# Performance work log

Hardware: AMD Instinct MI355X
Metric: run time of the kernel (lower is better)

## Reference

```python
import jax, jax.numpy as jnp
import numpy as np

N_NODES = 100000
N_EDGES = 300000
HIDDEN = 256

def _lin_init(key, fan_in, fan_out):
    return jax.random.normal(key, (fan_in, fan_out), jnp.float32) / np.sqrt(fan_in)

def setup_inputs():
    key = jax.random.key(0)
    ks = jax.random.split(key, 16)
    x = jax.random.randint(ks[0], (N_NODES, 16), 0, 11).astype(jnp.float32)
    edge_index = jax.random.randint(ks[1], (2, N_EDGES), 0, N_NODES)
    edge_attr = jax.random.randint(ks[2], (N_EDGES, 4), 0, 5).astype(jnp.float32)
    batch = jnp.sort(jax.random.randint(ks[3], (N_NODES,), 0, 256))
    atom_emb = jax.random.normal(ks[4], (11, 64), jnp.float32)
    bond_emb_table = jax.random.normal(ks[5], (5, 64), jnp.float32)
    vp_w1 = _lin_init(ks[6], 64, 32); vp_b1 = jnp.zeros((32,), jnp.float32)
    vp_w2 = _lin_init(ks[7], 32, 8)
    # chemical-knowledge bias init: max_valence - 1 for atom types 0..7 (bias dim is 8)
    vp_b2 = jnp.array([3., 2., 1., 5., 0., 0., 0., 0.], jnp.float32)
    gnn_wself = jax.random.normal(ks[8], (3, HIDDEN, HIDDEN), jnp.float32) / np.sqrt(HIDDEN)
    gnn_bself = jnp.zeros((3, HIDDEN), jnp.float32)
    gnn_wmsg = jax.random.normal(ks[9], (3, HIDDEN + 64, HIDDEN), jnp.float32) / np.sqrt(HIDDEN + 64)
    gnn_bmsg = jnp.zeros((3, HIDDEN), jnp.float32)
    bc_w1 = _lin_init(ks[10], 2 * HIDDEN + 2, 128); bc_b1 = jnp.zeros((128,), jnp.float32)
    bc_w2 = _lin_init(ks[11], 128, 64); bc_b2 = jnp.zeros((64,), jnp.float32)
    bc_w3 = _lin_init(ks[12], 64, 4); bc_b3 = jnp.zeros((4,), jnp.float32)
    cp_w1 = _lin_init(ks[13], HIDDEN, 128); cp_b1 = jnp.zeros((128,), jnp.float32)
    cp_w2 = _lin_init(ks[14], 128, 32); cp_b2 = jnp.zeros((32,), jnp.float32)
    return dict(x=x, edge_attr=edge_attr, atom_emb=atom_emb, bond_emb_table=bond_emb_table,
                vp_w1=vp_w1, vp_b1=vp_b1, vp_w2=vp_w2, vp_b2=vp_b2,
                gnn_wself=gnn_wself, gnn_bself=gnn_bself, gnn_wmsg=gnn_wmsg, gnn_bmsg=gnn_bmsg,
                bc_w1=bc_w1, bc_b1=bc_b1, bc_w2=bc_w2, bc_b2=bc_b2, bc_w3=bc_w3, bc_b3=bc_b3,
                cp_w1=cp_w1, cp_b1=cp_b1, cp_w2=cp_w2, cp_b2=cp_b2,
                edge_index=edge_index, batch=batch)

def _forward(x, edge_attr, atom_emb, bond_emb_table, vp_w1, vp_b1, vp_w2, vp_b2,
             gnn_wself, gnn_bself, gnn_wmsg, gnn_bmsg,
             bc_w1, bc_b1, bc_w2, bc_b2, bc_w3, bc_b3,
             cp_w1, cp_b1, cp_w2, cp_b2, edge_index, batch):
    relu = jax.nn.relu
    n = x.shape[0]
    atom_types = jnp.clip(x[:, 0].astype(jnp.int32), 0, 10)        # [N]
    ae = atom_emb[atom_types]                                      # [N, 64]
    valence_logits = relu(ae @ vp_w1 + vp_b1) @ vp_w2 + vp_b2      # [N, 8]
    pv = jnp.argmax(valence_logits, axis=-1) + 1                   # [N] predicted valences in [1,8]
    bt = jnp.clip(edge_attr[:, 0].astype(jnp.int32), 0, 4)
    be = bond_emb_table[bt]                                        # [E, 64]
    h = jnp.concatenate([ae, jax.nn.one_hot(pv - 1, 8, dtype=ae.dtype)], axis=-1)  # [N, 72]
    h = jnp.pad(h, ((0, 0), (0, HIDDEN - h.shape[1])))             # pad to [N, HIDDEN]
    row, col = edge_index[0], edge_index[1]
    # stacked ChemicalConstraintGNN layers (message passing with bond-type features)
    for l in range(3):
        msg = relu(jnp.concatenate([h[col], be], axis=-1) @ gnn_wmsg[l] + gnn_bmsg[l])  # [E, H]
        agg = jax.ops.segment_sum(msg, row, num_segments=n)
        h = relu(h @ gnn_wself[l] + gnn_bself[l] + agg)
    # ValenceConstraintLayer: damp nodes whose degree exceeds predicted valence
    degree = jax.ops.segment_sum(jnp.ones(row.shape[0], h.dtype), row, num_segments=n)
    violations = relu(degree - pv.astype(h.dtype))                 # [N]
    h = h / (1.0 + violations)[:, None]
    # constrained bond prediction
    bf = jnp.concatenate([h[row], h[col],
                          pv[row][:, None].astype(h.dtype), pv[col][:, None].astype(h.dtype)], axis=-1)
    bl = relu(relu(bf @ bc_w1 + bc_b1) @ bc_w2 + bc_b2) @ bc_w3 + bc_b3  # [E, 4]
    # vectorized chemical constraints (replaces per-edge Python loop)
    at_r, at_c = atom_types[row], atom_types[col]
    halogen = ((at_r == 4) | (at_r == 5) | (at_c == 4) | (at_c == 5)).astype(bl.dtype)
    lowval2 = ((pv[row] <= 2) | (pv[col] <= 2)).astype(bl.dtype)
    lowval1 = ((pv[row] <= 1) | (pv[col] <= 1)).astype(bl.dtype)
    penalty = jnp.zeros_like(bl)
    penalty = penalty.at[:, 1:].add((-100.0 * halogen - 50.0 * lowval1)[:, None])
    penalty = penalty.at[:, 2].add(-50.0 * lowval2)
    bond_logits = bl + penalty
    chem_props = relu(h @ cp_w1 + cp_b1) @ cp_w2 + cp_b2           # [N, 32]
    return h, chem_props, valence_logits, bond_logits, violations

def reference(x, edge_attr, atom_emb, bond_emb_table, vp_w1, vp_b1, vp_w2, vp_b2,
              gnn_wself, gnn_bself, gnn_wmsg, gnn_bmsg,
              bc_w1, bc_b1, bc_w2, bc_b2, bc_w3, bc_b3,
              cp_w1, cp_b1, cp_w2, cp_b2, edge_index, batch):
    return _forward(x, edge_attr, atom_emb, bond_emb_table, vp_w1, vp_b1, vp_w2, vp_b2,
                    gnn_wself, gnn_bself, gnn_wmsg, gnn_bmsg,
                    bc_w1, bc_b1, bc_w2, bc_b2, bc_w3, bc_b3,
                    cp_w1, cp_b1, cp_w2, cp_b2, edge_index, batch)
```

## Files before the change

### kernel.cpp

```cpp
#include <hip/hip_runtime.h>

#define N_NODES 100000
#define N_EDGES 300000
#define M_PAD   100096
#define E_PAD   300032

typedef unsigned short u16;
typedef short bf16x8 __attribute__((ext_vector_type(8)));
typedef float f32x4  __attribute__((ext_vector_type(4)));
typedef unsigned short u16x8 __attribute__((ext_vector_type(8)));

__device__ __forceinline__ float bf2f(u16 u) {
    unsigned x = ((unsigned)u) << 16;
    return __builtin_bit_cast(float, x);
}
__device__ __forceinline__ u16 f2bf(float f) {
    unsigned u = __builtin_bit_cast(unsigned, f);
    unsigned r = (u + 0x7FFF + ((u >> 16) & 1)) >> 16;
    return (u16)r;
}

#define H_OFF   0
#define CP_OFF  25600000
#define VL_OFF  28800000
#define BL_OFF  29600000
#define VI_OFF  30800000

#define GLL(gp, lp) __builtin_amdgcn_global_load_lds( \
    (const __attribute__((address_space(1))) unsigned int*)(gp), \
    (__attribute__((address_space(3))) unsigned int*)(lp), 16, 0, 0)

__global__ void k_type_mlp(const float* __restrict__ atom_emb,
                           const float* __restrict__ vp_w1, const float* __restrict__ vp_b1,
                           const float* __restrict__ vp_w2, const float* __restrict__ vp_b2,
                           const float* __restrict__ bself, const float* __restrict__ bcb1,
                           const float* __restrict__ cpb1,
                           int* __restrict__ pv_tab, float* __restrict__ vl_tab,
                           float* __restrict__ h0_tab,
                           float* __restrict__ bias512, float* __restrict__ biasPost)
{
    __shared__ float zs[11][32];
    __shared__ float lgs[11][8];
    int tid = threadIdx.x;
    for (int i = tid; i < 1024; i += 256) {
        int l = i >> 9, c = i & 511;
        bias512[l * 512 + c] = (c < 256) ? 0.f : bself[(l + 1) * 256 + (c - 256)];
    }
    for (int i = tid; i < 384; i += 256)
        biasPost[i] = (i < 128) ? bcb1[i] : ((i < 256) ? 0.f : cpb1[i - 256]);
    for (int i = tid; i < 11 * 256; i += 256) h0_tab[i] = 0.f;
    for (int u = tid; u < 352; u += 256) {
        int t = u >> 5, j = u & 31;
        const float* ae = atom_emb + t * 64;
        float z = vp_b1[j];
        for (int d = 0; d < 64; ++d) z += ae[d] * vp_w1[d * 32 + j];
        zs[t][j] = fmaxf(z, 0.f);
    }
    __syncthreads();
    if (tid < 88) {
        int t = tid >> 3, c = tid & 7;
        float lg = vp_b2[c];
        #pragma unroll
        for (int j = 0; j < 32; ++j) lg += zs[t][j] * vp_w2[j * 8 + c];
        lgs[t][c] = lg;
        vl_tab[t * 8 + c] = lg;
    }
    __syncthreads();
    if (tid < 11) {
        int t = tid;
        int best = 0;
        #pragma unroll
        for (int c = 1; c < 8; ++c) if (lgs[t][c] > lgs[t][best]) best = c;
        pv_tab[t] = best + 1;
        float* h0 = h0_tab + t * 256;
        const float* ae = atom_emb + t * 64;
        for (int d = 0; d < 64; ++d) h0[d] = ae[d];
        h0[64 + best] = 1.f;
    }
}

__global__ void k_tables(const float* __restrict__ bond_emb,
                         const float* __restrict__ gnn_wself, const float* __restrict__ gnn_bself,
                         const float* __restrict__ gnn_wmsg, const float* __restrict__ gnn_bmsg,
                         const float* __restrict__ h0_tab,
                         float* __restrict__ self0_tab, float* __restrict__ msg0_tab,
                         float* __restrict__ bondtab)
{
    int b = blockIdx.x, c = threadIdx.x;
    if (b < 11) {
        int t = b;
        const float* h0 = h0_tab + t * 256;
        float acc = gnn_bself[c];
        for (int k = 0; k < 256; ++k) acc += h0[k] * gnn_wself[k * 256 + c];
        self0_tab[t * 256 + c] = acc;
    } else if (b < 66) {
        int idx = b - 11; int t = idx / 5, bb = idx % 5;
        const float* h0 = h0_tab + t * 256;
        float acc = gnn_bmsg[c];
        for (int k = 0; k < 256; ++k) acc += h0[k] * gnn_wmsg[k * 256 + c];
        const float* be = bond_emb + bb * 64;
        for (int k = 0; k < 64; ++k) acc += be[k] * gnn_wmsg[(256 + k) * 256 + c];
        msg0_tab[idx * 256 + c] = fmaxf(acc, 0.f);
    } else {
        int idx = b - 66; int l = idx / 5 + 1, bb = idx % 5;
        const float* w = gnn_wmsg + (size_t)l * 320 * 256;
        const float* be = bond_emb + bb * 64;
        float acc = gnn_bmsg[l * 256 + c];
        for (int k = 0; k < 64; ++k) acc += be[k] * w[(256 + k) * 256 + c];
        bondtab[(l - 1) * 5 * 256 + bb * 256 + c] = acc;
    }
}

__global__ void k_wtrans(const float* __restrict__ wmsg, const float* __restrict__ wself,
                         const float* __restrict__ bcw1, const float* __restrict__ cpw1,
                         const float* __restrict__ bcw2, const float* __restrict__ cpw2,
                         u16* __restrict__ BtL1, u16* __restrict__ BtL2, u16* __restrict__ Bt3,
                         u16* __restrict__ BtW2, u16* __restrict__ BtCP2)
{
    int b = blockIdx.x, k = threadIdx.x;
    if (b < 512) {
        int n = b;
        float v = (n < 256) ? wmsg[(size_t)1 * 320 * 256 + (size_t)k * 256 + n]
                            : wself[(size_t)1 * 256 * 256 + (size_t)k * 256 + (n - 256)];
        BtL1[n * 256 + k] = f2bf(v);
    } else if (b < 1024) {
        int n = b - 512;
        float v = (n < 256) ? wmsg[(size_t)2 * 320 * 256 + (size_t)k * 256 + n]
                            : wself[(size_t)2 * 256 * 256 + (size_t)k * 256 + (n - 256)];
        BtL2[n * 256 + k] = f2bf(v);
    } else if (b < 1408) {
        int n = b - 1024;
        float v;
        if (n < 128)      v = bcw1[k * 128 + n];
        else if (n < 256) v = bcw1[(256 + k) * 128 + (n - 128)];
        else              v = cpw1[k * 128 + (n - 256)];
        Bt3[n * 256 + k] = f2bf(v);
    } else if (b < 1536) {
        int n = b - 1408;
        if (k < 128) BtW2[n * 128 + k] = f2bf(n < 64 ? bcw2[k * 64 + n] : 0.f);
    } else {
        int n = b - 1536;
        if (k < 128) BtCP2[n * 128 + k] = f2bf(n < 32 ? cpw2[k * 32 + n] : 0.f);
    }
}

#define NB_NODE ((N_NODES + 255) / 256)
#define NB_EDGE ((N_EDGES + 255) / 256)
__global__ void k_init_deg(const float* __restrict__ x, const int* __restrict__ pv_tab,
                           const float* __restrict__ vl_tab,
                           int* __restrict__ types, int* __restrict__ pvarr,
                           float* __restrict__ vl_out,
                           const int* __restrict__ ei, int* __restrict__ degree)
{
    int b = blockIdx.x;
    if (b < NB_NODE) {
        int i = b * 256 + threadIdx.x;
        if (i >= N_NODES) return;
        int t = (int)x[i * 16];
        t = min(max(t, 0), 10);
        types[i] = t;
        pvarr[i] = pv_tab[t];
        float4 v0 = *(const float4*)&vl_tab[t * 8];
        float4 v1 = *(const float4*)&vl_tab[t * 8 + 4];
        *(float4*)&vl_out[i * 8]     = v0;
        *(float4*)&vl_out[i * 8 + 4] = v1;
    } else {
        int e = (b - NB_NODE) * 256 + threadIdx.x;
        if (e >= N_EDGES) return;
        atomicAdd(&degree[ei[e]], 1);
    }
}

#define SCAN_B 1024
__global__ void k_scan1(const int* __restrict__ degree, int* __restrict__ part, int* __restrict__ bsum)
{
    __shared__ int s[SCAN_B];
    int tid = threadIdx.x;
    int i = blockIdx.x * SCAN_B + tid;
    int v = (i < N_NODES) ? degree[i] : 0;
    s[tid] = v; __syncthreads();
    for (int off = 1; off < SCAN_B; off <<= 1) {
        int t = (tid >= off) ? s[tid - off] : 0;
        __syncthreads();
        s[tid] += t;
        __syncthreads();
    }
    if (i < N_NODES) part[i] = s[tid] - v;
    if (tid == SCAN_B - 1) bsum[blockIdx.x] = s[tid];
}

__global__ void k_scan2(const int* __restrict__ bsum, int* __restrict__ bbase, int nb)
{
    __shared__ int s[128];
    int tid = threadIdx.x;
    int v = (tid < nb) ? bsum[tid] : 0;
    s[tid] = v; __syncthreads();
    for (int off = 1; off < 128; off <<= 1) {
        int t = (tid >= off) ? s[tid - off] : 0;
        __syncthreads();
        s[tid] += t;
        __syncthreads();
    }
    bbase[tid] = s[tid] - v;
}

__global__ void k_scan3(int* __restrict__ part, const int* __restrict__ bbase, int* __restrict__ cursor)
{
    int i = blockIdx.x * SCAN_B + threadIdx.x;
    if (i >= N_NODES) return;
    int o = part[i] + bbase[blockIdx.x];
    part[i] = o;
    cursor[i] = o;
}

__global__ void k_csr_fill(const int* __restrict__ ei, const float* __restrict__ edge_attr,
                           const int* __restrict__ types, int* __restrict__ cursor,
                           int* __restrict__ csr, int* __restrict__ rowcsr, int* __restrict__ eidarr)
{
    int e = blockIdx.x * blockDim.x + threadIdx.x;
    if (e >= N_EDGES) return;
    int row = ei[e], col = ei[N_EDGES + e];
    int bt = (int)edge_attr[e * 4];
    bt = min(max(bt, 0), 4);
    int pos = atomicAdd(&cursor[row], 1);
    csr[pos] = col | (bt << 20) | (types[col] << 24);
    rowcsr[pos] = row;
    eidarr[pos] = e;
}

__global__ __launch_bounds__(256) void k_agg0(const int* __restrict__ offsets, const int* __restrict__ degree,
                       const int* __restrict__ types,
                       const float* __restrict__ self0_tab, const float* __restrict__ msg0_tab,
                       const int* __restrict__ csr, u16* __restrict__ h)
{
    int wid = threadIdx.x >> 6, lane = threadIdx.x & 63;
    int node = blockIdx.x * 4 + wid;
    if (node >= N_NODES) return;
    int t = types[node];
    float4 acc = *(const float4*)&self0_tab[t * 256 + lane * 4];
    int start = offsets[node], deg = degree[node];
    int pj = (lane < deg) ? csr[start + lane] : 0;
    int dmax = min(deg, 64);
    for (int j = 0; j < dmax; ++j) {
        int p = __shfl(pj, j);
        int combo = ((p >> 24) & 0xF) * 5 + ((p >> 20) & 7);
        float4 m = *(const float4*)&msg0_tab[combo * 256 + lane * 4];
        acc.x += m.x; acc.y += m.y; acc.z += m.z; acc.w += m.w;
    }
    for (int j = 64; j < deg; ++j) {
        int p = csr[start + j];
        int combo = ((p >> 24) & 0xF) * 5 + ((p >> 20) & 7);
        float4 m = *(const float4*)&msg0_tab[combo * 256 + lane * 4];
        acc.x += m.x; acc.y += m.y; acc.z += m.z; acc.w += m.w;
    }
    ushort4 r;
    r.x = f2bf(fmaxf(acc.x, 0.f)); r.y = f2bf(fmaxf(acc.y, 0.f));
    r.z = f2bf(fmaxf(acc.z, 0.f)); r.w = f2bf(fmaxf(acc.w, 0.f));
    *(ushort4*)&h[(size_t)node * 256 + lane * 4] = r;
}

__global__ __launch_bounds__(256) void k_agg12(const int* __restrict__ offsets, const int* __restrict__ degree,
                        const u16* __restrict__ hs, const u16* __restrict__ hm,
                        const float* __restrict__ bondtab, const int* __restrict__ csr,
                        u16* __restrict__ h, int final_layer, const int* __restrict__ pvarr,
                        float* __restrict__ h_out, u16* __restrict__ hd_bf, float* __restrict__ viol_out)
{
    int wid = threadIdx.x >> 6, lane = threadIdx.x & 63;
    int node = blockIdx.x * 4 + wid;
    if (node >= N_NODES) return;
    ushort4 s4 = *(const ushort4*)&hs[(size_t)node * 256 + lane * 4];
    float ax = bf2f(s4.x), ay = bf2f(s4.y), az = bf2f(s4.z), aw = bf2f(s4.w);
    int start = offsets[node], deg = degree[node];
    int pj = (lane < deg) ? csr[start + lane] : 0;
    int dmax = min(deg, 64);
    if (dmax > 0) {
        int p0 = __shfl(pj, 0);
        ushort4 m0 = *(const ushort4*)&hm[(size_t)(p0 & 0xFFFFF) * 256 + lane * 4];
        for (int j = 1; j < dmax; ++j) {
            int p1 = __shfl(pj, j);
            ushort4 m1 = *(const ushort4*)&hm[(size_t)(p1 & 0xFFFFF) * 256 + lane * 4];
            float4 bb = *(const float4*)&bondtab[((p0 >> 20) & 7) * 256 + lane * 4];
            ax += fmaxf(bf2f(m0.x) + bb.x, 0.f);
            ay += fmaxf(bf2f(m0.y) + bb.y, 0.f);
            az += fmaxf(bf2f(m0.z) + bb.z, 0.f);
            aw += fmaxf(bf2f(m0.w) + bb.w, 0.f);
            m0 = m1; p0 = p1;
        }
        float4 bb = *(const float4*)&bondtab[((p0 >> 20) & 7) * 256 + lane * 4];
        ax += fmaxf(bf2f(m0.x) + bb.x, 0.f);
        ay += fmaxf(bf2f(m0.y) + bb.y, 0.f);
        az += fmaxf(bf2f(m0.z) + bb.z, 0.f);
        aw += fmaxf(bf2f(m0.w) + bb.w, 0.f);
    }
    for (int j = 64; j < deg; ++j) {
        int p = csr[start + j];
        int c = p & 0xFFFFF;
        int bt = (p >> 20) & 7;
        ushort4 m4 = *(const ushort4*)&hm[(size_t)c * 256 + lane * 4];
        float4 bb = *(const float4*)&bondtab[bt * 256 + lane * 4];
        ax += fmaxf(bf2f(m4.x) + bb.x, 0.f);
        ay += fmaxf(bf2f(m4.y) + bb.y, 0.f);
        az += fmaxf(bf2f(m4.z) + bb.z, 0.f);
        aw += fmaxf(bf2f(m4.w) + bb.w, 0.f);
    }
    ax = fmaxf(ax, 0.f); ay = fmaxf(ay, 0.f); az = fmaxf(az, 0.f); aw = fmaxf(aw, 0.f);
    if (!final_layer) {
        ushort4 r;
        r.x = f2bf(ax); r.y = f2bf(ay); r.z = f2bf(az); r.w = f2bf(aw);
        *(ushort4*)&h[(size_t)node * 256 + lane * 4] = r;
    } else {
        float viol = fmaxf((float)deg - (float)pvarr[node], 0.f);
        float s = 1.f / (1.f + viol);
        ax *= s; ay *= s; az *= s; aw *= s;
        float4 v = make_float4(ax, ay, az, aw);
        *(float4*)&h_out[(size_t)node * 256 + lane * 4] = v;
        ushort4 r;
        r.x = f2bf(ax); r.y = f2bf(ay); r.z = f2bf(az); r.w = f2bf(aw);
        *(ushort4*)&hd_bf[(size_t)node * 256 + lane * 4] = r;
        if (lane == 0) viol_out[node] = viol;
    }
}

__global__ __launch_bounds__(256) void k_gemm_dual(
    const u16* __restrict__ A, const u16* __restrict__ Bt,
    const float* __restrict__ bias512,
    u16* __restrict__ Dm, u16* __restrict__ Ds, int M, int MT)
{
    __shared__ u16 S[24576];
    u16* Cs = S;
    int b = blockIdx.x;
    int rsub = b & 31;
    int nt = rsub >> 3, m8 = rsub & 7;
    int mt = (b >> 5) * 8 + m8;
    if (mt >= MT) return;
    int bm = mt * 128, bn = nt * 128;

    int t = threadIdx.x;
    int lane = t & 63, w = t >> 6;
    int wm = w & 1, wn = w >> 1;
    f32x4 zero = {0.f, 0.f, 0.f, 0.f};
    f32x4 acc[4][4];
    #pragma unroll
    for (int i = 0; i < 4; ++i)
        #pragma unroll
        for (int j = 0; j < 4; ++j) acc[i][j] = zero;

    int arow = t >> 2, acol = (t & 3) * 8;
    const u16* Ag = A + (size_t)(bm + arow) * 256 + acol;
    const u16* Bg = Bt + (size_t)(bn + arow) * 256 + acol;
    int q = lane >> 4, r = lane & 15;

    GLL(Ag,                 S + t * 8);
    GLL(Ag + 64 * 256,      S + 2048 + t * 8);
    GLL(Bg,                 S + 4096 + t * 8);
    GLL(Bg + 64 * 256,      S + 4096 + 2048 + t * 8);
    GLL(Ag + 32,            S + 8192 + t * 8);
    GLL(Ag + 64 * 256 + 32, S + 8192 + 2048 + t * 8);
    GLL(Bg + 32,            S + 8192 + 4096 + t * 8);
    GLL(Bg + 64 * 256 + 32, S + 8192 + 4096 + 2048 + t * 8);

    #pragma unroll
    for (int ks = 0; ks < 8; ++ks) {
        int cb = (ks % 3) * 8192;
        if (ks < 7) {
            asm volatile("s_waitcnt vmcnt(4)" ::: "memory");
        } else {
            asm volatile("s_waitcnt vmcnt(0)" ::: "memory");
        }
        __builtin_amdgcn_s_barrier();
        __builtin_amdgcn_sched_barrier(0);
        if (ks < 6) {
            int nb = ((ks + 2) % 3) * 8192;
            int k0 = (ks + 2) * 32;
            GLL(Ag + k0,            S + nb + t * 8);
            GLL(Ag + 64 * 256 + k0, S + nb + 2048 + t * 8);
            GLL(Bg + k0,            S + nb + 4096 + t * 8);
            GLL(Bg + 64 * 256 + k0, S + nb + 4096 + 2048 + t * 8);
        }
        bf16x8 af[4], bfr[4];
        #pragma unroll
        for (int i = 0; i < 4; ++i)
            af[i] = *(const bf16x8*)&S[cb + (wm * 64 + i * 16 + r) * 32 + q * 8];
        #pragma unroll
        for (int j = 0; j < 4; ++j)
            bfr[j] = *(const bf16x8*)&S[cb + 4096 + (wn * 64 + j * 16 + r) * 32 + q * 8];
        __builtin_amdgcn_s_setprio(1);
        #pragma unroll
        for (int i = 0; i < 4; ++i)
            #pragma unroll
            for (int j = 0; j < 4; ++j)
                acc[i][j] = __builtin_amdgcn_mfma_f32_16x16x32_bf16(af[i], bfr[j], acc[i][j], 0, 0, 0);
        __builtin_amdgcn_s_setprio(0);
    }
    __syncthreads();

    #pragma unroll
    for (int i = 0; i < 4; ++i) {
        int rowl = wm * 64 + i * 16 + q * 4;
        #pragma unroll
        for (int j = 0; j < 4; ++j) {
            int coll = wn * 64 + j * 16 + r;
            float bv = bias512[bn + coll];
            #pragma unroll
            for (int rr = 0; rr < 4; ++rr)
                Cs[(rowl + rr) * 128 + coll] = f2bf(acc[i][j][rr] + bv);
        }
    }
    __syncthreads();
    u16* Dbase = (nt < 2) ? (Dm + bn) : (Ds + (bn - 256));
    int c16 = (t & 15) * 8, rbase = t >> 4;
    #pragma unroll
    for (int g = 0; g < 8; ++g) {
        int rowl = rbase + g * 16;
        int rowg = bm + rowl;
        if (rowg < M) {
            u16x8 v = *(const u16x8*)&Cs[rowl * 128 + c16];
            *(u16x8*)&Dbase[(size_t)rowg * 256 + c16] = v;
        }
    }
}

__global__ __launch_bounds__(256) void k_gemm_post(
    const u16* __restrict__ A, const u16* __restrict__ Bt3,
    const float* __restrict__ biasPost,
    u16* __restrict__ UV, const u16* __restrict__ BtCP2, const float* __restrict__ cp_b2,
    float* __restrict__ CPOUT, int M, int MT)
{
    __shared__ u16 S[24576];
    u16* Cs = S;
    int b = blockIdx.x;
    int rsub = b % 24;
    int nt = rsub >> 3, m8 = rsub & 7;
    int mt = (b / 24) * 8 + m8;
    if (mt >= MT) return;
    int bm = mt * 128, bn = nt * 128;

    int t = threadIdx.x;
    int lane = t & 63, w = t >> 6;
    int wm = w & 1, wn = w >> 1;
    f32x4 zero = {0.f, 0.f, 0.f, 0.f};
    f32x4 acc[4][4];
    #pragma unroll
    for (int i = 0; i < 4; ++i)
        #pragma unroll
        for (int j = 0; j < 4; ++j) acc[i][j] = zero;

    int arow = t >> 2, acol = (t & 3) * 8;
    const u16* Ag = A + (size_t)(bm + arow) * 256 + acol;
    const u16* Bg = Bt3 + (size_t)(bn + arow) * 256 + acol;
    int q = lane >> 4, r = lane & 15;

    GLL(Ag,                 S + t * 8);
    GLL(Ag + 64 * 256,      S + 2048 + t * 8);
    GLL(Bg,                 S + 4096 + t * 8);
    GLL(Bg + 64 * 256,      S + 4096 + 2048 + t * 8);
    GLL(Ag + 32,            S + 8192 + t * 8);
    GLL(Ag + 64 * 256 + 32, S + 8192 + 2048 + t * 8);
    GLL(Bg + 32,            S + 8192 + 4096 + t * 8);
    GLL(Bg + 64 * 256 + 32, S + 8192 + 4096 + 2048 + t * 8);

    #pragma unroll
    for (int ks = 0; ks < 8; ++ks) {
        int cb = (ks % 3) * 8192;
        if (ks < 7) {
            asm volatile("s_waitcnt vmcnt(4)" ::: "memory");
        } else {
            asm volatile("s_waitcnt vmcnt(0)" ::: "memory");
        }
        __builtin_amdgcn_s_barrier();
        __builtin_amdgcn_sched_barrier(0);
        if (ks < 6) {
            int nb = ((ks + 2) % 3) * 8192;
            int k0 = (ks + 2) * 32;
            GLL(Ag + k0,            S + nb + t * 8);
            GLL(Ag + 64 * 256 + k0, S + nb + 2048 + t * 8);
            GLL(Bg + k0,            S + nb + 4096 + t * 8);
            GLL(Bg + 64 * 256 + k0, S + nb + 4096 + 2048 + t * 8);
        }
        bf16x8 af[4], bfr[4];
        #pragma unroll
        for (int i = 0; i < 4; ++i)
            af[i] = *(const bf16x8*)&S[cb + (wm * 64 + i * 16 + r) * 32 + q * 8];
        #pragma unroll
        for (int j = 0; j < 4; ++j)
            bfr[j] = *(const bf16x8*)&S[cb + 4096 + (wn * 64 + j * 16 + r) * 32 + q * 8];
        __builtin_amdgcn_s_setprio(1);
        #pragma unroll
        for (int i = 0; i < 4; ++i)
            #pragma unroll
            for (int j = 0; j < 4; ++j)
                acc[i][j] = __builtin_amdgcn_mfma_f32_16x16x32_bf16(af[i], bfr[j], acc[i][j], 0, 0, 0);
        __builtin_amdgcn_s_setprio(0);
    }
    __syncthreads();

    #pragma unroll
    for (int i = 0; i < 4; ++i) {
        int rowl = wm * 64 + i * 16 + q * 4;
        #pragma unroll
        for (int j = 0; j < 4; ++j) {
            int coll = wn * 64 + j * 16 + r;
            float bv = biasPost[bn + coll];
            #pragma unroll
            for (int rr = 0; rr < 4; ++rr) {
                float val = acc[i][j][rr] + bv;
                if (nt == 2) val = fmaxf(val, 0.f);
                Cs[(rowl + rr) * 128 + coll] = f2bf(val);
            }
        }
    }
    __syncthreads();
    if (nt < 2) {
        int c16 = (t & 15) * 8, rbase = t >> 4;
        #pragma unroll
        for (int g = 0; g < 8; ++g) {
            int rowl = rbase + g * 16;
            int rowg = bm + rowl;
            if (rowg < M) {
                u16x8 v = *(const u16x8*)&Cs[rowl * 128 + c16];
                *(u16x8*)&UV[(size_t)rowg * 256 + bn + c16] = v;
            }
        }
    } else if (wn < 2) {
        f32x4 a2[4];
        #pragma unroll
        for (int i = 0; i < 4; ++i) a2[i] = zero;
        #pragma unroll
        for (int kc = 0; kc < 4; ++kc) {
            bf16x8 af2[4];
            #pragma unroll
            for (int i = 0; i < 4; ++i)
                af2[i] = *(const bf16x8*)&Cs[(wm * 64 + i * 16 + r) * 128 + kc * 32 + q * 8];
            bf16x8 bfr2 = *(const bf16x8*)&BtCP2[(size_t)(wn * 16 + r) * 128 + kc * 32 + q * 8];
            #pragma unroll
            for (int i = 0; i < 4; ++i)
                a2[i] = __builtin_amdgcn_mfma_f32_16x16x32_bf16(af2[i], bfr2, a2[i], 0, 0, 0);
        }
        int colg = wn * 16 + r;
        float bv2 = cp_b2[colg];
        #pragma unroll
        for (int i = 0; i < 4; ++i) {
            #pragma unroll
            for (int rr = 0; rr < 4; ++rr) {
                int rowg = bm + wm * 64 + i * 16 + q * 4 + rr;
                if (rowg < M) CPOUT[(size_t)rowg * 32 + colg] = a2[i][rr] + bv2;
            }
        }
    }
}

__global__ __launch_bounds__(256) void k_bond_fused(
    const int* __restrict__ csr, const int* __restrict__ rowcsr, const int* __restrict__ eidarr,
    const int* __restrict__ types, const int* __restrict__ pvarr, const int* __restrict__ pv_tab,
    const u16* __restrict__ uv, const float* __restrict__ bc_w1,
    const u16* __restrict__ BtW2, const float* __restrict__ bc_b2,
    const float* __restrict__ bc_w3, const float* __restrict__ bc_b3,
    float* __restrict__ bl_out)
{
    __shared__ u16 T1s[16384];
    __shared__ u16 Bs[16384];
    __shared__ float w5s[128], w6s[128], W3s[256], b2s[64], b3s[4];
    __shared__ int pvts[16];

    int t = threadIdx.x;
    int p0 = blockIdx.x * 128;

    if (t < 128) { w5s[t] = bc_w1[512 * 128 + t]; w6s[t] = bc_w1[513 * 128 + t]; }
    if (t < 256) W3s[t] = bc_w3[t];
    if (t < 64) b2s[t] = bc_b2[t];
    if (t < 4)  b3s[t] = bc_b3[t];
    if (t < 11) pvts[t] = pv_tab[t];
    #pragma unroll
    for (int c = 0; c < 4; ++c) {
        GLL(BtW2 + (size_t)(t >> 2) * 128 + c * 32 + (t & 3) * 8,        Bs + c * 4096 + t * 8);
        GLL(BtW2 + (size_t)(64 + (t >> 2)) * 128 + c * 32 + (t & 3) * 8, Bs + c * 4096 + 2048 + t * 8);
    }

    int l = t >> 1;
    int half = t & 1;
    int pos = p0 + l;
    int prow = 0, pk = 0;
    if (pos < N_EDGES) { prow = rowcsr[pos]; pk = csr[pos]; }
    int pcol = pk & 0xFFFFF;
    float pvr = (float)pvarr[prow];
    __syncthreads();
    float pvc = (float)pvts[(pk >> 24) & 0xF];

    const u16* up = uv + (size_t)prow * 256 + half * 64;
    const u16* vp = uv + (size_t)pcol * 256 + 128 + half * 64;
    #pragma unroll
    for (int j = 0; j < 8; ++j) {
        int c = half * 64 + j * 8;
        u16x8 uu = *(const u16x8*)(up + j * 8);
        u16x8 vv = *(const u16x8*)(vp + j * 8);
        int chunk = c >> 5, kk = c & 31;
        u16x8 o;
        #pragma unroll
        for (int e = 0; e < 8; ++e)
            o[e] = f2bf(fmaxf(bf2f(uu[e]) + bf2f(vv[e]) + pvr * w5s[c + e] + pvc * w6s[c + e], 0.f));
        *(u16x8*)(T1s + chunk * 4096 + l * 32 + kk) = o;
    }
    __syncthreads();

    int lane = t & 63, w = t >> 6;
    int wm = w & 1, wn = w >> 1;
    int q = lane >> 4, r = lane & 15;
    f32x4 zero = {0.f, 0.f, 0.f, 0.f};
    f32x4 acc[4][4];
    #pragma unroll
    for (int i = 0; i < 4; ++i)
        #pragma unroll
        for (int j = 0; j < 4; ++j) acc[i][j] = zero;
    #pragma unroll
    for (int c = 0; c < 4; ++c) {
        bf16x8 af[4], bfr[4];
        #pragma unroll
        for (int i = 0; i < 4; ++i)
            af[i] = *(const bf16x8*)&T1s[c * 4096 + (wm * 64 + i * 16 + r) * 32 + q * 8];
        #pragma unroll
        for (int j = 0; j < 4; ++j)
            bfr[j] = *(const bf16x8*)&Bs[c * 4096 + (wn * 64 + j * 16 + r) * 32 + q * 8];
        #pragma unroll
        for (int i = 0; i < 4; ++i)
            #pragma unroll
            for (int j = 0; j < 4; ++j)
                acc[i][j] = __builtin_amdgcn_mfma_f32_16x16x32_bf16(af[i], bfr[j], acc[i][j], 0, 0, 0);
    }
    __syncthreads();

    float* T2f = (float*)T1s;
    if (wn == 0) {
        #pragma unroll
        for (int i = 0; i < 4; ++i) {
            int row = wm * 64 + i * 16 + q * 4;
            #pragma unroll
            for (int j = 0; j < 4; ++j) {
                int col = j * 16 + r;
                float bv = b2s[col];
                #pragma unroll
                for (int rr = 0; rr < 4; ++rr)
                    T2f[(row + rr) * 64 + col] = fmaxf(acc[i][j][rr] + bv, 0.f);
            }
        }
    }
    __syncthreads();

    if (t < 128) {
        int pos3 = p0 + t;
        if (pos3 < N_EDGES) {
            float a0 = b3s[0], a1 = b3s[1], a2 = b3s[2], a3 = b3s[3];
            const float* trow = &T2f[t * 64];
            #pragma unroll 8
            for (int kk = 0; kk < 64; ++kk) {
                int k = (kk + t) & 63;
                float tv = trow[k];
                float4 w3 = *(const float4*)&W3s[k * 4];
                a0 += tv * w3.x;
                a1 += tv * w3.y;
                a2 += tv * w3.z;
                a3 += tv * w3.w;
            }
            int prow3 = rowcsr[pos3];
            int pk3 = csr[pos3];
            int tc = (pk3 >> 24) & 0xF;
            int tr = types[prow3];
            int pr = pvarr[prow3];
            int pc = pvts[tc];
            float halogen = (tr == 4 || tr == 5 || tc == 4 || tc == 5) ? 1.f : 0.f;
            float l1 = (pr <= 1 || pc <= 1) ? 1.f : 0.f;
            float l2 = (pr <= 2 || pc <= 2) ? 1.f : 0.f;
            float pen13 = -100.f * halogen - 50.f * l1;
            a1 += pen13;
            a3 += pen13;
            a2 += pen13 - 50.f * l2;
            int eid = eidarr[pos3];
            *(float4*)&bl_out[(size_t)eid * 4] = make_float4(a0, a1, a2, a3);
        }
    }
}

extern "C" void kernel_launch(void* const* d_in, const int* in_sizes, int n_in,
                              void* d_out, int out_size, void* d_ws, size_t ws_size,
                              hipStream_t stream)
{
    const float* x          = (const float*)d_in[0];
    const float* edge_attr  = (const float*)d_in[1];
    const float* atom_emb   = (const float*)d_in[2];
    const float* bond_emb   = (const float*)d_in[3];
    const float* vp_w1      = (const float*)d_in[4];
    const float* vp_b1      = (const float*)d_in[5];
    const float* vp_w2      = (const float*)d_in[6];
    const float* vp_b2      = (const float*)d_in[7];
    const float* gnn_wself  = (const float*)d_in[8];
    const float* gnn_bself  = (const float*)d_in[9];
    const float* gnn_wmsg   = (const float*)d_in[10];
    const float* gnn_bmsg   = (const float*)d_in[11];
    const float* bc_w1      = (const float*)d_in[12];
    const float* bc_b1      = (const float*)d_in[13];
    const float* bc_w2      = (const float*)d_in[14];
    const float* bc_b2      = (const float*)d_in[15];
    const float* bc_w3      = (const float*)d_in[16];
    const float* bc_b3      = (const float*)d_in[17];
    const float* cp_w1      = (const float*)d_in[18];
    const float* cp_b1      = (const float*)d_in[19];
    const float* cp_w2      = (const float*)d_in[20];
    const float* cp_b2      = (const float*)d_in[21];
    const int*   ei         = (const int*)d_in[22];

    float* out    = (float*)d_out;
    float* h_out  = out + H_OFF;
    float* cp_out = out + CP_OFF;
    float* vl_out = out + VL_OFF;
    float* bl_out = out + BL_OFF;
    float* vi_out = out + VI_OFF;

    char* base = (char*)d_ws;
    const size_t S = (size_t)M_PAD * 256 * 2;
    u16* h_bf  = (u16*)(base + 0 * S);
    u16* uv_bf = (u16*)(base + 0 * S);
    u16* hm_bf = (u16*)(base + 1 * S);
    u16* hs_bf = (u16*)(base + 2 * S);
    u16* hd_bf = (u16*)(base + 3 * S);
    u16* cp1_bf= (u16*)(base + 4 * S);
    char* w    = base + 4 * S + (size_t)M_PAD * 128 * 2;
    int* degree  = (int*)w; w += (size_t)N_NODES * 4;
    int* offsets = (int*)w; w += (size_t)N_NODES * 4;
    int* cursor  = (int*)w; w += (size_t)N_NODES * 4;
    int* types   = (int*)w; w += (size_t)N_NODES * 4;
    int* pvarr   = (int*)w; w += (size_t)N_NODES * 4;
    int* csr     = (int*)w; w += (size_t)E_PAD * 4;
    int* rowcsr  = (int*)w; w += (size_t)E_PAD * 4;
    int* eidarr  = (int*)w; w += (size_t)E_PAD * 4;
    int* bsum    = (int*)w; w += 4096;
    int* bbase   = (int*)w; w += 4096;
    int* pv_tab  = (int*)w; w += 1024;
    float* vl_tab    = (float*)w; w += 2048;
    float* h0_tab    = (float*)w; w += 11 * 256 * 4;
    float* self0_tab = (float*)w; w += 11 * 256 * 4;
    float* msg0_tab  = (float*)w; w += 55 * 256 * 4;
    float* bondtab   = (float*)w; w += 2 * 5 * 256 * 4;
    u16* BtL1  = (u16*)w; w += 512 * 256 * 2;
    u16* BtL2  = (u16*)w; w += 512 * 256 * 2;
    u16* Bt3   = (u16*)w; w += 384 * 256 * 2;
    u16* BtW2  = (u16*)w; w += 128 * 128 * 2;
    u16* BtCP2 = (u16*)w; w += 128 * 128 * 2;
    float* bias512  = (float*)w; w += 2 * 512 * 4;
    float* biasPost = (float*)w; w += 384 * 4;

    hipMemsetAsync(degree, 0, (size_t)N_NODES * 4, stream);
    k_type_mlp<<<1, 256, 0, stream>>>(atom_emb, vp_w1, vp_b1, vp_w2, vp_b2,
                                      gnn_bself, bc_b1, cp_b1,
                                      pv_tab, vl_tab, h0_tab, bias512, biasPost);
    k_tables<<<76, 256, 0, stream>>>(bond_emb, gnn_wself, gnn_bself, gnn_wmsg, gnn_bmsg,
                                     h0_tab, self0_tab, msg0_tab, bondtab);
    k_wtrans<<<1664, 256, 0, stream>>>(gnn_wmsg, gnn_wself, bc_w1, cp_w1, bc_w2, cp_w2,
                                       BtL1, BtL2, Bt3, BtW2, BtCP2);
    k_init_deg<<<NB_NODE + NB_EDGE, 256, 0, stream>>>(x, pv_tab, vl_tab, types, pvarr, vl_out, ei, degree);
    int nb = (N_NODES + SCAN_B - 1) / SCAN_B;
    k_scan1<<<nb, SCAN_B, 0, stream>>>(degree, offsets, bsum);
    k_scan2<<<1, 128, 0, stream>>>(bsum, bbase, nb);
    k_scan3<<<nb, SCAN_B, 0, stream>>>(offsets, bbase, cursor);
    k_csr_fill<<<(N_EDGES + 255) / 256, 256, 0, stream>>>(ei, edge_attr, types, cursor, csr, rowcsr, eidarr);
    k_agg0<<<N_NODES / 4, 256, 0, stream>>>(offsets, degree, types, self0_tab, msg0_tab, csr, h_bf);

    const int MT = M_PAD / 128;
    const int QB = (MT + 7) / 8;
    for (int l = 1; l <= 2; ++l) {
        const u16* BtL = (l == 1) ? BtL1 : BtL2;
        k_gemm_dual<<<QB * 32, 256, 0, stream>>>(h_bf, BtL, bias512 + (size_t)(l - 1) * 512,
                                                 hm_bf, hs_bf, N_NODES, MT);
        k_agg12<<<N_NODES / 4, 256, 0, stream>>>(offsets, degree, hs_bf, hm_bf,
                                                 bondtab + (size_t)(l - 1) * 5 * 256, csr, h_bf,
                                                 (l == 2) ? 1 : 0, pvarr, h_out, hd_bf, vi_out);
    }

    k_gemm_post<<<QB * 24, 256, 0, stream>>>(hd_bf, Bt3, biasPost, uv_bf, BtCP2, cp_b2, cp_out, N_NODES, MT);

    k_bond_fused<<<E_PAD / 128, 256, 0, stream>>>(csr, rowcsr, eidarr, types, pvarr, pv_tab,
                                                  uv_bf, bc_w1, BtW2, bc_b2, bc_w3, bc_b3, bl_out);
}
```

Before: 550.1 us.

## Merge setup kernels, tile weight transposes, and fold block-sum scan into scan3

```diff
diff --git a/kernel.cpp b/kernel.cpp
--- a/kernel.cpp
+++ b/kernel.cpp
@@ -79,68 +79,88 @@
     }
 }
 
-__global__ void k_tables(const float* __restrict__ bond_emb,
+__global__ void k_setup2(const float* __restrict__ bond_emb,
                          const float* __restrict__ gnn_wself, const float* __restrict__ gnn_bself,
                          const float* __restrict__ gnn_wmsg, const float* __restrict__ gnn_bmsg,
                          const float* __restrict__ h0_tab,
                          float* __restrict__ self0_tab, float* __restrict__ msg0_tab,
-                         float* __restrict__ bondtab)
-{
-    int b = blockIdx.x, c = threadIdx.x;
-    if (b < 11) {
-        int t = b;
-        const float* h0 = h0_tab + t * 256;
-        float acc = gnn_bself[c];
-        for (int k = 0; k < 256; ++k) acc += h0[k] * gnn_wself[k * 256 + c];
-        self0_tab[t * 256 + c] = acc;
-    } else if (b < 66) {
-        int idx = b - 11; int t = idx / 5, bb = idx % 5;
-        const float* h0 = h0_tab + t * 256;
-        float acc = gnn_bmsg[c];
-        for (int k = 0; k < 256; ++k) acc += h0[k] * gnn_wmsg[k * 256 + c];
-        const float* be = bond_emb + bb * 64;
-        for (int k = 0; k < 64; ++k) acc += be[k] * gnn_wmsg[(256 + k) * 256 + c];
-        msg0_tab[idx * 256 + c] = fmaxf(acc, 0.f);
-    } else {
-        int idx = b - 66; int l = idx / 5 + 1, bb = idx % 5;
-        const float* w = gnn_wmsg + (size_t)l * 320 * 256;
-        const float* be = bond_emb + bb * 64;
-        float acc = gnn_bmsg[l * 256 + c];
-        for (int k = 0; k < 64; ++k) acc += be[k] * w[(256 + k) * 256 + c];
-        bondtab[(l - 1) * 5 * 256 + bb * 256 + c] = acc;
-    }
-}
-
-__global__ void k_wtrans(const float* __restrict__ wmsg, const float* __restrict__ wself,
+                         float* __restrict__ bondtab,
                          const float* __restrict__ bcw1, const float* __restrict__ cpw1,
                          const float* __restrict__ bcw2, const float* __restrict__ cpw2,
                          u16* __restrict__ BtL1, u16* __restrict__ BtL2, u16* __restrict__ Bt3,
                          u16* __restrict__ BtW2, u16* __restrict__ BtCP2)
 {
-    int b = blockIdx.x, k = threadIdx.x;
-    if (b < 512) {
-        int n = b;
-        float v = (n < 256) ? wmsg[(size_t)1 * 320 * 256 + (size_t)k * 256 + n]
-                            : wself[(size_t)1 * 256 * 256 + (size_t)k * 256 + (n - 256)];
-        BtL1[n * 256 + k] = f2bf(v);
-    } else if (b < 1024) {
-        int n = b - 512;
-        float v = (n < 256) ? wmsg[(size_t)2 * 320 * 256 + (size_t)k * 256 + n]
-                            : wself[(size_t)2 * 256 * 256 + (size_t)k * 256 + (n - 256)];
-        BtL2[n * 256 + k] = f2bf(v);
-    } else if (b < 1408) {
-        int n = b - 1024;
-        float v;
-        if (n < 128)      v = bcw1[k * 128 + n];
-        else if (n < 256) v = bcw1[(256 + k) * 128 + (n - 128)];
-        else              v = cpw1[k * 128 + (n - 256)];
-        Bt3[n * 256 + k] = f2bf(v);
-    } else if (b < 1536) {
-        int n = b - 1408;
-        if (k < 128) BtW2[n * 128 + k] = f2bf(n < 64 ? bcw2[k * 64 + n] : 0.f);
+    int b = blockIdx.x;
+    int t = threadIdx.x;
+    if (b < 76) {
+        int c = t;
+        if (b < 11) {
+            int ty = b;
+            const float* h0 = h0_tab + ty * 256;
+            float acc = gnn_bself[c];
+            for (int k = 0; k < 256; ++k) acc += h0[k] * gnn_wself[k * 256 + c];
+            self0_tab[ty * 256 + c] = acc;
+        } else if (b < 66) {
+            int idx = b - 11; int ty = idx / 5, bb = idx % 5;
+            const float* h0 = h0_tab + ty * 256;
+            float acc = gnn_bmsg[c];
+            for (int k = 0; k < 256; ++k) acc += h0[k] * gnn_wmsg[k * 256 + c];
+            const float* be = bond_emb + bb * 64;
+            for (int k = 0; k < 64; ++k) acc += be[k] * gnn_wmsg[(256 + k) * 256 + c];
+            msg0_tab[idx * 256 + c] = fmaxf(acc, 0.f);
+        } else {
+            int idx = b - 66; int l = idx / 5 + 1, bb = idx % 5;
+            const float* w = gnn_wmsg + (size_t)l * 320 * 256;
+            const float* be = bond_emb + bb * 64;
+            float acc = gnn_bmsg[l * 256 + c];
+            for (int k = 0; k < 64; ++k) acc += be[k] * w[(256 + k) * 256 + c];
+            bondtab[(l - 1) * 5 * 256 + bb * 256 + c] = acc;
+        }
+    } else if (b < 164) {
+        __shared__ float tile[64][65];
+        int tt = b - 76;
+        u16* dst;
+        int n0, k0;
+        const float* srcbase;
+        int ld, noff;
+        if (tt < 64) {
+            int l = (tt < 32) ? 1 : 2;
+            int q = tt & 31;
+            dst = (l == 1) ? BtL1 : BtL2;
+            n0 = (q >> 2) * 64; k0 = (q & 3) * 64;
+            if (n0 < 256) { srcbase = gnn_wmsg + (size_t)l * 320 * 256; ld = 256; noff = n0; }
+            else          { srcbase = gnn_wself + (size_t)l * 256 * 256; ld = 256; noff = n0 - 256; }
+        } else {
+            int q = tt - 64;
+            dst = Bt3;
+            n0 = (q >> 2) * 64; k0 = (q & 3) * 64;
+            if (n0 < 128)      { srcbase = bcw1;             ld = 128; noff = n0; }
+            else if (n0 < 256) { srcbase = bcw1 + 256 * 128; ld = 128; noff = n0 - 128; }
+            else               { srcbase = cpw1;             ld = 128; noff = n0 - 256; }
+        }
+        int tn = t & 63, tq = t >> 6;
+        #pragma unroll
+        for (int i = 0; i < 16; ++i) {
+            int tk = tq * 16 + i;
+            tile[tk][tn] = srcbase[(size_t)(k0 + tk) * ld + noff + tn];
+        }
+        __syncthreads();
+        int tk2 = t & 63;
+        #pragma unroll
+        for (int i = 0; i < 16; ++i) {
+            int tn2 = tq * 16 + i;
+            dst[(size_t)(n0 + tn2) * 256 + k0 + tk2] = f2bf(tile[tk2][tn2]);
+        }
     } else {
-        int n = b - 1536;
-        if (k < 128) BtCP2[n * 128 + k] = f2bf(n < 32 ? cpw2[k * 32 + n] : 0.f);
+        int bb = b - 164;
+        int k = t;
+        if (bb < 128) {
+            int n = bb;
+            if (k < 128) BtW2[n * 128 + k] = f2bf(n < 64 ? bcw2[k * 64 + n] : 0.f);
+        } else {
+            int n = bb - 128;
+            if (k < 128) BtCP2[n * 128 + k] = f2bf(n < 32 ? cpw2[k * 32 + n] : 0.f);
+        }
     }
 }
 
@@ -189,26 +209,24 @@
     if (tid == SCAN_B - 1) bsum[blockIdx.x] = s[tid];
 }
 
-__global__ void k_scan2(const int* __restrict__ bsum, int* __restrict__ bbase, int nb)
+__global__ void k_scan3(int* __restrict__ part, const int* __restrict__ bsum,
+                        int* __restrict__ cursor, int nb)
 {
     __shared__ int s[128];
     int tid = threadIdx.x;
-    int v = (tid < nb) ? bsum[tid] : 0;
-    s[tid] = v; __syncthreads();
+    if (tid < 128) s[tid] = (tid < nb) ? bsum[tid] : 0;
+    __syncthreads();
     for (int off = 1; off < 128; off <<= 1) {
-        int t = (tid >= off) ? s[tid - off] : 0;
+        int v = 0;
+        if (tid < 128 && tid >= off) v = s[tid - off];
         __syncthreads();
-        s[tid] += t;
+        if (tid < 128) s[tid] += v;
         __syncthreads();
     }
-    bbase[tid] = s[tid] - v;
-}
-
-__global__ void k_scan3(int* __restrict__ part, const int* __restrict__ bbase, int* __restrict__ cursor)
-{
-    int i = blockIdx.x * SCAN_B + threadIdx.x;
+    int base = (blockIdx.x == 0) ? 0 : s[blockIdx.x - 1];
+    int i = blockIdx.x * SCAN_B + tid;
     if (i >= N_NODES) return;
-    int o = part[i] + bbase[blockIdx.x];
+    int o = part[i] + base;
     part[i] = o;
     cursor[i] = o;
 }
@@ -751,15 +769,14 @@
     k_type_mlp<<<1, 256, 0, stream>>>(atom_emb, vp_w1, vp_b1, vp_w2, vp_b2,
                                       gnn_bself, bc_b1, cp_b1,
                                       pv_tab, vl_tab, h0_tab, bias512, biasPost);
-    k_tables<<<76, 256, 0, stream>>>(bond_emb, gnn_wself, gnn_bself, gnn_wmsg, gnn_bmsg,
-                                     h0_tab, self0_tab, msg0_tab, bondtab);
-    k_wtrans<<<1664, 256, 0, stream>>>(gnn_wmsg, gnn_wself, bc_w1, cp_w1, bc_w2, cp_w2,
-                                       BtL1, BtL2, Bt3, BtW2, BtCP2);
+    k_setup2<<<420, 256, 0, stream>>>(bond_emb, gnn_wself, gnn_bself, gnn_wmsg, gnn_bmsg,
+                                      h0_tab, self0_tab, msg0_tab, bondtab,
+                                      bc_w1, cp_w1, bc_w2, cp_w2,
+                                      BtL1, BtL2, Bt3, BtW2, BtCP2);
     k_init_deg<<<NB_NODE + NB_EDGE, 256, 0, stream>>>(x, pv_tab, vl_tab, types, pvarr, vl_out, ei, degree);
     int nb = (N_NODES + SCAN_B - 1) / SCAN_B;
     k_scan1<<<nb, SCAN_B, 0, stream>>>(degree, offsets, bsum);
-    k_scan2<<<1, 128, 0, stream>>>(bsum, bbase, nb);
-    k_scan3<<<nb, SCAN_B, 0, stream>>>(offsets, bbase, cursor);
+    k_scan3<<<nb, SCAN_B, 0, stream>>>(offsets, bsum, cursor, nb);
     k_csr_fill<<<(N_EDGES + 255) / 256, 256, 0, stream>>>(ei, edge_attr, types, cursor, csr, rowcsr, eidarr);
     k_agg0<<<N_NODES / 4, 256, 0, stream>>>(offsets, degree, types, self0_tab, msg0_tab, csr, h_bf);
 
```

After: 545.0 us. About the same (-0.9%).
